# Kernel optimization log

Hardware: AMD Instinct MI355X
Metric: run time of the kernel (lower is better)

The kernel has to match this reference:

```python
import jax, jax.numpy as jnp
import numpy as np

B, H, W, K, A = 4096, 32, 32, 20, 4


def setup_inputs() -> dict:
    key = jax.random.key(0)
    k_wall, k_agent, k_goal, k_phi, k_l1, k_l2 = jax.random.split(key, 6)
    # obs channels: 0 = wall/feature map (random), 1 = one-hot agent pos, 2 = one-hot goal pos
    walls = jax.random.uniform(k_wall, (B, H, W), dtype=jnp.float32)
    agent_idx = jax.random.randint(k_agent, (B,), 0, H * W)
    goal_idx = jax.random.randint(k_goal, (B,), 0, H * W)
    agent = jax.nn.one_hot(agent_idx, H * W, dtype=jnp.float32).reshape(B, H, W)
    goal = jax.nn.one_hot(goal_idx, H * W, dtype=jnp.float32).reshape(B, H, W)
    obs = jnp.stack([walls, agent, goal], axis=-1)  # (B,H,W,3)
    obs_flat = obs.reshape(B, H * W * 3)
    din = H * W * 3
    return {
        "obs_flat": obs_flat,
        "Phi_w": jax.random.normal(k_phi, (din, 2 * H * W), dtype=jnp.float32) * 0.02,
        "Phi_b": jnp.zeros((2 * H * W,), jnp.float32),
        "L1_w": jax.random.normal(k_l1, (36, 16), dtype=jnp.float32) * 0.1,
        "L1_b": jnp.zeros((16,), jnp.float32),
        "L2_w": jax.random.normal(k_l2, (16, A), dtype=jnp.float32) * 0.1,
        "L2_b": jnp.zeros((A,), jnp.float32),
    }


def _mvprop(r, p):
    # K-step value propagation: V <- max(V, r + p*(best 4-neighbor V - r))
    # p = sigmoid(...) >= 0, so max over the 4 shifted nv values equals nv of the max shift.
    def body(V, _):
        pv = jnp.pad(V, ((0, 0), (1, 1), (1, 1)))
        nbr = jnp.maximum(
            jnp.maximum(pv[:, :-2, 1:-1], pv[:, 2:, 1:-1]),   # up, down
            jnp.maximum(pv[:, 1:-1, :-2], pv[:, 1:-1, 2:]),   # left, right
        )
        return jnp.maximum(V, r + p * (nbr - r)), None
    V, _ = jax.lax.scan(body, r, None, length=K)
    return V


def reference(obs_flat, Phi_w, Phi_b, L1_w, L1_b, L2_w, L2_b):
    b = obs_flat.shape[0]
    obs = obs_flat.reshape(b, H, W, 3)
    phi = jax.nn.sigmoid(obs_flat @ Phi_w + Phi_b).reshape(b, H, W, 2)
    r, p = phi[..., 0], phi[..., 1]
    V = _mvprop(r, p)  # (b,H,W)
    obs_val = jnp.concatenate([obs, V[..., None]], axis=-1)  # (b,H,W,4)
    padded = jnp.pad(obs_val, ((0, 0), (1, 1), (1, 1), (0, 0)))
    # agent position: exactly one nonzero in channel 1 per sample -> argmax
    idx = jnp.argmax(obs[..., 1].reshape(b, -1), axis=1)
    pi, pj = idx // W, idx % W
    # 3x3 neighborhood around agent in padded grid (start = pos+1-1 = pos)
    def slice_one(ov, i, j):
        return jax.lax.dynamic_slice(ov, (i, j, 0), (3, 3, 4))
    sel = jax.vmap(slice_one)(padded, pi, pj)  # (b,3,3,4)
    h = jax.nn.relu(sel.reshape(b, 36) @ L1_w + L1_b)
    logit = h @ L2_w + L2_b
    return logit
```

## Files before the change

### kernel.cpp

```cpp
#include <hip/hip_runtime.h>
#include <hip/hip_fp16.h>

#define BATCH 4096
#define HH 32
#define WW 32
#define KPROP 20
#define NACT 4
#define DIN 3072
#define DPHI 2048
#define HWC 1024
#define KC 1024

typedef _Float16 h8_t __attribute__((ext_vector_type(8)));
typedef _Float16 h4_t __attribute__((ext_vector_type(4)));
typedef float f32x4 __attribute__((ext_vector_type(4)));

__device__ inline void load_lds16(const _Float16* g, _Float16* l) {
    __builtin_amdgcn_global_load_lds(
        (const __attribute__((address_space(1))) void*)g,
        (__attribute__((address_space(3))) void*)l, 16, 0, 0);
}

__device__ inline float sigmoidf(float x) { return 1.0f / (1.0f + __expf(-x)); }

__global__ __launch_bounds__(256) void prep_kernel(
    const float* __restrict__ obs,
    _Float16* __restrict__ W16,
    int* __restrict__ aidx, int* __restrict__ gidx)
{
    const int t = blockIdx.x * 256 + threadIdx.x;
    const int b = t >> 8;
    const int c0 = (t & 255) * 4;
    const float* src = obs + (size_t)b * DIN + 3 * c0;
    const float4 f0 = *(const float4*)(src);
    const float4 f1 = *(const float4*)(src + 4);
    const float4 f2 = *(const float4*)(src + 8);
    h4_t w;
    w[0] = (_Float16)f0.x; w[1] = (_Float16)f0.w;
    w[2] = (_Float16)f1.z; w[3] = (_Float16)f2.y;
    *(h4_t*)(W16 + (size_t)b * KC + c0) = w;
    if (f0.y > 0.5f) aidx[b] = c0;
    if (f1.x > 0.5f) aidx[b] = c0 + 1;
    if (f1.w > 0.5f) aidx[b] = c0 + 2;
    if (f2.z > 0.5f) aidx[b] = c0 + 3;
    if (f0.z > 0.5f) gidx[b] = c0;
    if (f1.y > 0.5f) gidx[b] = c0 + 1;
    if (f2.x > 0.5f) gidx[b] = c0 + 2;
    if (f2.w > 0.5f) gidx[b] = c0 + 3;
}

__global__ __launch_bounds__(256) void transpose_kernel(
    const float* __restrict__ Phi_w,
    _Float16* __restrict__ PwT)
{
    __shared__ float tile[32][33];
    const int tx = threadIdx.x & 31;
    const int ty = threadIdx.x >> 5;
    const int ci = blockIdx.y;
    const int ni = blockIdx.x;
    #pragma unroll
    for (int s = 0; s < 4; s++) {
        const int r = ty + 8 * s;
        tile[r][tx] = Phi_w[(size_t)(3 * (ci * 32 + r)) * DPHI + ni * 32 + tx];
    }
    __syncthreads();
    #pragma unroll
    for (int s = 0; s < 4; s++) {
        const int r = ty + 8 * s;
        PwT[(size_t)(ni * 32 + r) * KC + ci * 32 + tx] = (_Float16)tile[tx][r];
    }
}

#define BM 128
#define BN 128

__global__ __launch_bounds__(256) void gemm_pre_kernel(
    const _Float16* __restrict__ A,
    const _Float16* __restrict__ Bt,
    const float* __restrict__ bias,
    _Float16* __restrict__ pre)
{
    __shared__ _Float16 As2[4 * BM * 8];
    __shared__ _Float16 Bs2[4 * BN * 8];

    const int tid  = threadIdx.x;
    const int lane = tid & 63;
    const int wid  = tid >> 6;
    const int m0 = blockIdx.y * BM;
    const int n0 = blockIdx.x * BN;
    const int wm = (wid >> 1) * 64;
    const int wn = (wid & 1) * 64;
    const int lm = lane & 15;
    const int kq = lane >> 4;

    f32x4 acc[4][4] = {};

    const int sm  = tid & 127;
    const int sk0 = tid >> 7;
    const _Float16* Abase = A  + (size_t)(m0 + sm) * KC;
    const _Float16* Bbase = Bt + (size_t)(n0 + sm) * KC;

    for (int k0 = 0; k0 < KC; k0 += 32) {
        #pragma unroll
        for (int r2 = 0; r2 < 2; r2++) {
            const int kqs = sk0 + 2 * r2;
            load_lds16(Abase + k0 + kqs * 8, As2 + (tid + 256 * r2) * 8);
            load_lds16(Bbase + k0 + kqs * 8, Bs2 + (tid + 256 * r2) * 8);
        }
        __syncthreads();

        h8_t af[4], bf[4];
        #pragma unroll
        for (int mt = 0; mt < 4; mt++)
            af[mt] = *(const h8_t*)(As2 + (kq * BM + wm + mt * 16 + lm) * 8);
        #pragma unroll
        for (int nt = 0; nt < 4; nt++)
            bf[nt] = *(const h8_t*)(Bs2 + (kq * BN + wn + nt * 16 + lm) * 8);

        #pragma unroll
        for (int mt = 0; mt < 4; mt++)
            #pragma unroll
            for (int nt = 0; nt < 4; nt++)
                acc[mt][nt] = __builtin_amdgcn_mfma_f32_16x16x32_f16(
                    af[mt], bf[nt], acc[mt][nt], 0, 0, 0);
        __syncthreads();
    }

    #pragma unroll
    for (int nt = 0; nt < 4; nt++) {
        const int col = n0 + wn + nt * 16 + lm;
        const float bcol = bias[col];
        #pragma unroll
        for (int mt = 0; mt < 4; mt++) {
            #pragma unroll
            for (int r = 0; r < 4; r++) {
                const int row = m0 + wm + mt * 16 + kq * 4 + r;
                pre[(size_t)row * DPHI + col] = (_Float16)(acc[mt][nt][r] + bcol);
            }
        }
    }
}

__global__ __launch_bounds__(256) void vprop_head_kernel(
    const _Float16* __restrict__ pre,
    const float* __restrict__ Phi_w,
    const float* __restrict__ obs,
    const int* __restrict__ aidx,
    const int* __restrict__ gidx,
    const float* __restrict__ L1w,
    const float* __restrict__ L1b,
    const float* __restrict__ L2w,
    const float* __restrict__ L2b,
    float* __restrict__ out)
{
    __shared__ __align__(16) float VB[2][34 * 40];
    __shared__ float sel[36], hbuf[16];

    const int b = blockIdx.x;
    const int tid = threadIdx.x;
    const int ai = aidx[b];
    const int gi = gidx[b];

    for (int idx = tid; idx < 2 * 34 * 40; idx += 256)
        ((float*)VB)[idx] = 0.0f;

    const h8_t ph = *(const h8_t*)(pre + (size_t)b * DPHI + 8 * tid);
    const float* rA = Phi_w + (size_t)(3 * ai + 1) * DPHI + 8 * tid;
    const float* rG = Phi_w + (size_t)(3 * gi + 2) * DPHI + 8 * tid;
    const float4 a0 = *(const float4*)(rA);
    const float4 a1 = *(const float4*)(rA + 4);
    const float4 g0 = *(const float4*)(rG);
    const float4 g1 = *(const float4*)(rG + 4);
    float v[8];
    v[0] = (float)ph[0] + a0.x + g0.x;  v[1] = (float)ph[1] + a0.y + g0.y;
    v[2] = (float)ph[2] + a0.z + g0.z;  v[3] = (float)ph[3] + a0.w + g0.w;
    v[4] = (float)ph[4] + a1.x + g1.x;  v[5] = (float)ph[5] + a1.y + g1.y;
    v[6] = (float)ph[6] + a1.z + g1.z;  v[7] = (float)ph[7] + a1.w + g1.w;

    float4 vR, pp, aR;
    vR.x = sigmoidf(v[0]); pp.x = sigmoidf(v[1]);
    vR.y = sigmoidf(v[2]); pp.y = sigmoidf(v[3]);
    vR.z = sigmoidf(v[4]); pp.z = sigmoidf(v[5]);
    vR.w = sigmoidf(v[6]); pp.w = sigmoidf(v[7]);
    aR.x = vR.x * (1.0f - pp.x); aR.y = vR.y * (1.0f - pp.y);
    aR.z = vR.z * (1.0f - pp.z); aR.w = vR.w * (1.0f - pp.w);

    const int i = tid >> 3;
    const int q = tid & 7;
    const int rowoff = (i + 1) * 40 + 4 + 4 * q;

    __syncthreads();
    *(float4*)&VB[0][rowoff] = vR;
    __syncthreads();

    int cur = 0;
    for (int it = 0; it < KPROP; it++) {
        const float* Vold = VB[cur];
        float* Vnew = VB[1 - cur];
        const float4 up = *(const float4*)&Vold[rowoff - 40];
        const float4 dn = *(const float4*)&Vold[rowoff + 40];
        const float lf = Vold[rowoff - 1];
        const float rt = Vold[rowoff + 4];
        float4 nb;
        nb.x = fmaxf(fmaxf(up.x, dn.x), fmaxf(lf,   vR.y));
        nb.y = fmaxf(fmaxf(up.y, dn.y), fmaxf(vR.x, vR.z));
        nb.z = fmaxf(fmaxf(up.z, dn.z), fmaxf(vR.y, vR.w));
        nb.w = fmaxf(fmaxf(up.w, dn.w), fmaxf(vR.z, rt));
        vR.x = fmaxf(vR.x, aR.x + pp.x * nb.x);
        vR.y = fmaxf(vR.y, aR.y + pp.y * nb.y);
        vR.z = fmaxf(vR.z, aR.z + pp.z * nb.z);
        vR.w = fmaxf(vR.w, aR.w + pp.w * nb.w);
        *(float4*)&Vnew[rowoff] = vR;
        __syncthreads();
        cur ^= 1;
    }

    const int pi = ai >> 5, pj = ai & 31;
    if (tid < 36) {
        const int cell = tid >> 2;
        const int ch = tid & 3;
        const int di = pi + cell / 3 - 1;
        const int dj = pj + cell % 3 - 1;
        float vv;
        if (ch == 3) {
            vv = VB[cur][(di + 1) * 40 + 4 + dj];
        } else {
            vv = 0.0f;
            if (di >= 0 && di < HH && dj >= 0 && dj < WW)
                vv = obs[(size_t)b * DIN + (di * WW + dj) * 3 + ch];
        }
        sel[tid] = vv;
    }
    __syncthreads();

    if (tid < 16) {
        float h = L1b[tid];
        #pragma unroll
        for (int k = 0; k < 36; k++) h += sel[k] * L1w[k * 16 + tid];
        hbuf[tid] = fmaxf(h, 0.0f);
    }
    __syncthreads();

    if (tid < 4) {
        float o = L2b[tid];
        #pragma unroll
        for (int t = 0; t < 16; t++) o += hbuf[t] * L2w[t * 4 + tid];
        out[(size_t)b * NACT + tid] = o;
    }
}

extern "C" void kernel_launch(void* const* d_in, const int* in_sizes, int n_in,
                              void* d_out, int out_size, void* d_ws, size_t ws_size,
                              hipStream_t stream) {
    const float* obs   = (const float*)d_in[0];
    const float* Phi_w = (const float*)d_in[1];
    const float* Phi_b = (const float*)d_in[2];
    const float* L1w   = (const float*)d_in[3];
    const float* L1b   = (const float*)d_in[4];
    const float* L2w   = (const float*)d_in[5];
    const float* L2b   = (const float*)d_in[6];
    float* out = (float*)d_out;

    char* ws = (char*)d_ws;
    _Float16* pre = (_Float16*)ws;
    _Float16* W16 = (_Float16*)(ws + 16777216);
    _Float16* PwT = (_Float16*)(ws + 16777216 + 8388608);
    int* aidx = (int*)(ws + 29360128);
    int* gidx = aidx + BATCH;

    prep_kernel<<<BATCH, 256, 0, stream>>>(obs, W16, aidx, gidx);
    transpose_kernel<<<dim3(64, 32), 256, 0, stream>>>(Phi_w, PwT);
    gemm_pre_kernel<<<dim3(DPHI / BN, BATCH / BM), 256, 0, stream>>>(W16, PwT, Phi_b, pre);
    vprop_head_kernel<<<BATCH, 256, 0, stream>>>(pre, Phi_w, obs, aidx, gidx,
                                                 L1w, L1b, L2w, L2b, out);
}
```

Baseline: 182.2 us.

## Run value propagation per wavefront in registers and double-buffer GEMM LDS

The value-propagation kernel now maps one sample to one 64-lane wavefront, with four samples per block. Each lane keeps a 2x8 patch of the grid in registers and trades halos with DPP row shifts and shuffles, which removes the per-iteration LDS round trips and block-wide barriers. The agent and goal rows of Phi_w are copied to an fp16 gather table during weight prep, and the GEMM double-buffers its LDS tiles so it needs one barrier per k-step instead of two. The risks are a small precision change from the fp16 agent/goal rows and higher register pressure in the propagation kernel.

```diff
diff --git a/kernel.cpp b/kernel.cpp
--- a/kernel.cpp
+++ b/kernel.cpp
@@ -22,6 +22,15 @@
 }
 
 __device__ inline float sigmoidf(float x) { return 1.0f / (1.0f + __expf(-x)); }
+
+__device__ inline float dpp_shr1(float x) {
+    return __int_as_float(__builtin_amdgcn_update_dpp(
+        0, __float_as_int(x), 0x111, 0xF, 0xF, true));
+}
+__device__ inline float dpp_shl1(float x) {
+    return __int_as_float(__builtin_amdgcn_update_dpp(
+        0, __float_as_int(x), 0x101, 0xF, 0xF, true));
+}
 
 __global__ __launch_bounds__(256) void prep_kernel(
     const float* __restrict__ obs,
@@ -49,9 +58,10 @@
     if (f2.w > 0.5f) gidx[b] = c0 + 3;
 }
 
-__global__ __launch_bounds__(256) void transpose_kernel(
+__global__ __launch_bounds__(256) void wprep_kernel(
     const float* __restrict__ Phi_w,
-    _Float16* __restrict__ PwT)
+    _Float16* __restrict__ PwT,
+    _Float16* __restrict__ Pag)
 {
     __shared__ float tile[32][33];
     const int tx = threadIdx.x & 31;
@@ -61,7 +71,11 @@
     #pragma unroll
     for (int s = 0; s < 4; s++) {
         const int r = ty + 8 * s;
-        tile[r][tx] = Phi_w[(size_t)(3 * (ci * 32 + r)) * DPHI + ni * 32 + tx];
+        const int c = ci * 32 + r;
+        const int n = ni * 32 + tx;
+        tile[r][tx] = Phi_w[(size_t)(3 * c) * DPHI + n];
+        Pag[(size_t)c * DPHI + n]                      = (_Float16)Phi_w[(size_t)(3 * c + 1) * DPHI + n];
+        Pag[(size_t)(HWC + c) * DPHI + n]              = (_Float16)Phi_w[(size_t)(3 * c + 2) * DPHI + n];
     }
     __syncthreads();
     #pragma unroll
@@ -73,6 +87,17 @@
 
 #define BM 128
 #define BN 128
+
+__device__ inline void stage_tile(const _Float16* Abase, const _Float16* Bbase, int k0,
+                                  _Float16* As, _Float16* Bs, int tid) {
+    const int sk0 = tid >> 7;
+    #pragma unroll
+    for (int r2 = 0; r2 < 2; r2++) {
+        const int kqs = sk0 + 2 * r2;
+        load_lds16(Abase + k0 + kqs * 8, As + (tid + 256 * r2) * 8);
+        load_lds16(Bbase + k0 + kqs * 8, Bs + (tid + 256 * r2) * 8);
+    }
+}
 
 __global__ __launch_bounds__(256) void gemm_pre_kernel(
     const _Float16* __restrict__ A,
@@ -80,8 +105,8 @@
     const float* __restrict__ bias,
     _Float16* __restrict__ pre)
 {
-    __shared__ _Float16 As2[4 * BM * 8];
-    __shared__ _Float16 Bs2[4 * BN * 8];
+    __shared__ _Float16 As[2][4 * BM * 8];
+    __shared__ _Float16 Bs[2][4 * BN * 8];
 
     const int tid  = threadIdx.x;
     const int lane = tid & 63;
@@ -95,27 +120,25 @@
 
     f32x4 acc[4][4] = {};
 
-    const int sm  = tid & 127;
-    const int sk0 = tid >> 7;
+    const int sm = tid & 127;
     const _Float16* Abase = A  + (size_t)(m0 + sm) * KC;
     const _Float16* Bbase = Bt + (size_t)(n0 + sm) * KC;
 
+    stage_tile(Abase, Bbase, 0, As[0], Bs[0], tid);
+
+    int cur = 0;
     for (int k0 = 0; k0 < KC; k0 += 32) {
-        #pragma unroll
-        for (int r2 = 0; r2 < 2; r2++) {
-            const int kqs = sk0 + 2 * r2;
-            load_lds16(Abase + k0 + kqs * 8, As2 + (tid + 256 * r2) * 8);
-            load_lds16(Bbase + k0 + kqs * 8, Bs2 + (tid + 256 * r2) * 8);
-        }
         __syncthreads();
+        if (k0 + 32 < KC)
+            stage_tile(Abase, Bbase, k0 + 32, As[cur ^ 1], Bs[cur ^ 1], tid);
 
         h8_t af[4], bf[4];
         #pragma unroll
         for (int mt = 0; mt < 4; mt++)
-            af[mt] = *(const h8_t*)(As2 + (kq * BM + wm + mt * 16 + lm) * 8);
+            af[mt] = *(const h8_t*)(As[cur] + (kq * BM + wm + mt * 16 + lm) * 8);
         #pragma unroll
         for (int nt = 0; nt < 4; nt++)
-            bf[nt] = *(const h8_t*)(Bs2 + (kq * BN + wn + nt * 16 + lm) * 8);
+            bf[nt] = *(const h8_t*)(Bs[cur] + (kq * BN + wn + nt * 16 + lm) * 8);
 
         #pragma unroll
         for (int mt = 0; mt < 4; mt++)
@@ -123,7 +146,7 @@
             for (int nt = 0; nt < 4; nt++)
                 acc[mt][nt] = __builtin_amdgcn_mfma_f32_16x16x32_f16(
                     af[mt], bf[nt], acc[mt][nt], 0, 0, 0);
-        __syncthreads();
+        cur ^= 1;
     }
 
     #pragma unroll
@@ -141,9 +164,9 @@
     }
 }
 
-__global__ __launch_bounds__(256) void vprop_head_kernel(
+__global__ __launch_bounds__(256, 4) void vprop_head_kernel(
     const _Float16* __restrict__ pre,
-    const float* __restrict__ Phi_w,
+    const _Float16* __restrict__ Pag,
     const float* __restrict__ obs,
     const int* __restrict__ aidx,
     const int* __restrict__ gidx,
@@ -153,99 +176,110 @@
     const float* __restrict__ L2b,
     float* __restrict__ out)
 {
-    __shared__ __align__(16) float VB[2][34 * 40];
-    __shared__ float sel[36], hbuf[16];
-
-    const int b = blockIdx.x;
-    const int tid = threadIdx.x;
+    __shared__ __align__(16) float Vg[4][HWC];
+    __shared__ float sel[4][36], hbuf[4][16];
+
+    const int tid  = threadIdx.x;
+    const int w    = tid >> 6;
+    const int lane = tid & 63;
+    const int b    = blockIdx.x * 4 + w;
+    const int bi   = lane & 15;
+    const int bj   = lane >> 4;
     const int ai = aidx[b];
     const int gi = gidx[b];
 
-    for (int idx = tid; idx < 2 * 34 * 40; idx += 256)
-        ((float*)VB)[idx] = 0.0f;
-
-    const h8_t ph = *(const h8_t*)(pre + (size_t)b * DPHI + 8 * tid);
-    const float* rA = Phi_w + (size_t)(3 * ai + 1) * DPHI + 8 * tid;
-    const float* rG = Phi_w + (size_t)(3 * gi + 2) * DPHI + 8 * tid;
-    const float4 a0 = *(const float4*)(rA);
-    const float4 a1 = *(const float4*)(rA + 4);
-    const float4 g0 = *(const float4*)(rG);
-    const float4 g1 = *(const float4*)(rG + 4);
-    float v[8];
-    v[0] = (float)ph[0] + a0.x + g0.x;  v[1] = (float)ph[1] + a0.y + g0.y;
-    v[2] = (float)ph[2] + a0.z + g0.z;  v[3] = (float)ph[3] + a0.w + g0.w;
-    v[4] = (float)ph[4] + a1.x + g1.x;  v[5] = (float)ph[5] + a1.y + g1.y;
-    v[6] = (float)ph[6] + a1.z + g1.z;  v[7] = (float)ph[7] + a1.w + g1.w;
-
-    float4 vR, pp, aR;
-    vR.x = sigmoidf(v[0]); pp.x = sigmoidf(v[1]);
-    vR.y = sigmoidf(v[2]); pp.y = sigmoidf(v[3]);
-    vR.z = sigmoidf(v[4]); pp.z = sigmoidf(v[5]);
-    vR.w = sigmoidf(v[6]); pp.w = sigmoidf(v[7]);
-    aR.x = vR.x * (1.0f - pp.x); aR.y = vR.y * (1.0f - pp.y);
-    aR.z = vR.z * (1.0f - pp.z); aR.w = vR.w * (1.0f - pp.w);
-
-    const int i = tid >> 3;
-    const int q = tid & 7;
-    const int rowoff = (i + 1) * 40 + 4 + 4 * q;
-
+    const _Float16* pb = pre + (size_t)b * DPHI;
+    const _Float16* ra = Pag + (size_t)ai * DPHI;
+    const _Float16* rg = Pag + (size_t)(HWC + gi) * DPHI;
+
+    float v[2][8], p[2][8], a[2][8];
+    #pragma unroll
+    for (int r = 0; r < 2; r++) {
+        const int off = 64 * (2 * bi + r) + 16 * bj;
+        const h8_t ph0 = *(const h8_t*)(pb + off), ph1 = *(const h8_t*)(pb + off + 8);
+        const h8_t pa0 = *(const h8_t*)(ra + off), pa1 = *(const h8_t*)(ra + off + 8);
+        const h8_t pg0 = *(const h8_t*)(rg + off), pg1 = *(const h8_t*)(rg + off + 8);
+        #pragma unroll
+        for (int c = 0; c < 4; c++) {
+            const float rv = sigmoidf((float)ph0[2*c]   + (float)pa0[2*c]   + (float)pg0[2*c]);
+            const float pv = sigmoidf((float)ph0[2*c+1] + (float)pa0[2*c+1] + (float)pg0[2*c+1]);
+            v[r][c] = rv; p[r][c] = pv; a[r][c] = rv * (1.0f - pv);
+            const float rv2 = sigmoidf((float)ph1[2*c]   + (float)pa1[2*c]   + (float)pg1[2*c]);
+            const float pv2 = sigmoidf((float)ph1[2*c+1] + (float)pa1[2*c+1] + (float)pg1[2*c+1]);
+            v[r][c+4] = rv2; p[r][c+4] = pv2; a[r][c+4] = rv2 * (1.0f - pv2);
+        }
+    }
+
+    for (int it = 0; it < KPROP; it++) {
+        float uh[8], dh[8], lh[2], rh[2];
+        #pragma unroll
+        for (int c = 0; c < 8; c++) {
+            uh[c] = dpp_shr1(v[1][c]);
+            dh[c] = dpp_shl1(v[0][c]);
+        }
+        #pragma unroll
+        for (int r = 0; r < 2; r++) {
+            lh[r] = __shfl(v[r][7], lane - 16);
+            rh[r] = __shfl(v[r][0], lane + 16);
+            if (bj == 0) lh[r] = 0.0f;
+            if (bj == 3) rh[r] = 0.0f;
+        }
+        float nb[2][8];
+        #pragma unroll
+        for (int c = 0; c < 8; c++) {
+            const float lf0 = (c == 0) ? lh[0] : v[0][c-1];
+            const float rt0 = (c == 7) ? rh[0] : v[0][c+1];
+            const float lf1 = (c == 0) ? lh[1] : v[1][c-1];
+            const float rt1 = (c == 7) ? rh[1] : v[1][c+1];
+            nb[0][c] = fmaxf(fmaxf(uh[c], v[1][c]), fmaxf(lf0, rt0));
+            nb[1][c] = fmaxf(fmaxf(v[0][c], dh[c]), fmaxf(lf1, rt1));
+        }
+        #pragma unroll
+        for (int r = 0; r < 2; r++)
+            #pragma unroll
+            for (int c = 0; c < 8; c++)
+                v[r][c] = fmaxf(v[r][c], fmaf(p[r][c], nb[r][c], a[r][c]));
+    }
+
+    #pragma unroll
+    for (int r = 0; r < 2; r++) {
+        float4 lo, hi;
+        lo.x = v[r][0]; lo.y = v[r][1]; lo.z = v[r][2]; lo.w = v[r][3];
+        hi.x = v[r][4]; hi.y = v[r][5]; hi.z = v[r][6]; hi.w = v[r][7];
+        const int base = (2 * bi + r) * 32 + 8 * bj;
+        *(float4*)&Vg[w][base]     = lo;
+        *(float4*)&Vg[w][base + 4] = hi;
+    }
     __syncthreads();
-    *(float4*)&VB[0][rowoff] = vR;
-    __syncthreads();
-
-    int cur = 0;
-    for (int it = 0; it < KPROP; it++) {
-        const float* Vold = VB[cur];
-        float* Vnew = VB[1 - cur];
-        const float4 up = *(const float4*)&Vold[rowoff - 40];
-        const float4 dn = *(const float4*)&Vold[rowoff + 40];
-        const float lf = Vold[rowoff - 1];
-        const float rt = Vold[rowoff + 4];
-        float4 nb;
-        nb.x = fmaxf(fmaxf(up.x, dn.x), fmaxf(lf,   vR.y));
-        nb.y = fmaxf(fmaxf(up.y, dn.y), fmaxf(vR.x, vR.z));
-        nb.z = fmaxf(fmaxf(up.z, dn.z), fmaxf(vR.y, vR.w));
-        nb.w = fmaxf(fmaxf(up.w, dn.w), fmaxf(vR.z, rt));
-        vR.x = fmaxf(vR.x, aR.x + pp.x * nb.x);
-        vR.y = fmaxf(vR.y, aR.y + pp.y * nb.y);
-        vR.z = fmaxf(vR.z, aR.z + pp.z * nb.z);
-        vR.w = fmaxf(vR.w, aR.w + pp.w * nb.w);
-        *(float4*)&Vnew[rowoff] = vR;
-        __syncthreads();
-        cur ^= 1;
-    }
 
     const int pi = ai >> 5, pj = ai & 31;
-    if (tid < 36) {
-        const int cell = tid >> 2;
-        const int ch = tid & 3;
+    if (lane < 36) {
+        const int cell = lane >> 2;
+        const int ch = lane & 3;
         const int di = pi + cell / 3 - 1;
         const int dj = pj + cell % 3 - 1;
-        float vv;
-        if (ch == 3) {
-            vv = VB[cur][(di + 1) * 40 + 4 + dj];
-        } else {
-            vv = 0.0f;
-            if (di >= 0 && di < HH && dj >= 0 && dj < WW)
-                vv = obs[(size_t)b * DIN + (di * WW + dj) * 3 + ch];
-        }
-        sel[tid] = vv;
+        float vv = 0.0f;
+        if (di >= 0 && di < HH && dj >= 0 && dj < WW) {
+            const int c = di * WW + dj;
+            vv = (ch < 3) ? obs[(size_t)b * DIN + 3 * c + ch] : Vg[w][c];
+        }
+        sel[w][lane] = vv;
     }
     __syncthreads();
 
-    if (tid < 16) {
-        float h = L1b[tid];
-        #pragma unroll
-        for (int k = 0; k < 36; k++) h += sel[k] * L1w[k * 16 + tid];
-        hbuf[tid] = fmaxf(h, 0.0f);
+    if (lane < 16) {
+        float h = L1b[lane];
+        #pragma unroll
+        for (int k = 0; k < 36; k++) h += sel[w][k] * L1w[k * 16 + lane];
+        hbuf[w][lane] = fmaxf(h, 0.0f);
     }
     __syncthreads();
 
-    if (tid < 4) {
-        float o = L2b[tid];
-        #pragma unroll
-        for (int t = 0; t < 16; t++) o += hbuf[t] * L2w[t * 4 + tid];
-        out[(size_t)b * NACT + tid] = o;
+    if (lane < 4) {
+        float o = L2b[lane];
+        #pragma unroll
+        for (int t = 0; t < 16; t++) o += hbuf[w][t] * L2w[t * 4 + lane];
+        out[(size_t)b * NACT + lane] = o;
     }
 }
 
@@ -264,13 +298,14 @@
     char* ws = (char*)d_ws;
     _Float16* pre = (_Float16*)ws;
     _Float16* W16 = (_Float16*)(ws + 16777216);
-    _Float16* PwT = (_Float16*)(ws + 16777216 + 8388608);
-    int* aidx = (int*)(ws + 29360128);
+    _Float16* PwT = (_Float16*)(ws + 25165824);
+    _Float16* Pag = (_Float16*)(ws + 29360128);
+    int* aidx = (int*)(ws + 37748736);
     int* gidx = aidx + BATCH;
 
     prep_kernel<<<BATCH, 256, 0, stream>>>(obs, W16, aidx, gidx);
-    transpose_kernel<<<dim3(64, 32), 256, 0, stream>>>(Phi_w, PwT);
+    wprep_kernel<<<dim3(64, 32), 256, 0, stream>>>(Phi_w, PwT, Pag);
     gemm_pre_kernel<<<dim3(DPHI / BN, BATCH / BM), 256, 0, stream>>>(W16, PwT, Phi_b, pre);
-    vprop_head_kernel<<<BATCH, 256, 0, stream>>>(pre, Phi_w, obs, aidx, gidx,
-                                                 L1w, L1b, L2w, L2b, out);
-}
+    vprop_head_kernel<<<BATCH / 4, 256, 0, stream>>>(pre, Pag, obs, aidx, gidx,
+                                                     L1w, L1b, L2w, L2b, out);
+}
```

After: 178.5 us. -2.1%, faster.
